# Kernel tuning notes

Hardware: AMD Instinct MI355X
Metric: run time of the kernel (lower is better)

Reference implementation:

```python
import jax, jax.numpy as jnp
import numpy as np

T_VALUES = [0.015, 0.06, 0.25, 1.0]
EPS = 1e-05
SR_OVER_HOP = 44100.0 / 512.0  # frames per second


def _s_values():
    t = np.asarray(T_VALUES, dtype=np.float32) * SR_OVER_HOP
    s = (np.sqrt(1.0 + 4.0 * t ** 2) - 1.0) / (2.0 * t ** 2)
    return jnp.asarray(s, dtype=jnp.float32)  # (n_s,)


def setup_inputs() -> dict:
    key = jax.random.key(0)
    k1, = jax.random.split(key, 1)
    B, F, T = 16, 128, 4096
    # non-negative energies (spectrogram magnitudes)
    x = jax.random.uniform(k1, (B, F, T), dtype=jnp.float32) * 10.0
    alpha_log = jnp.full((F,), float(np.log(0.8)), dtype=jnp.float32)
    delta_log = jnp.full((F,), float(np.log(10.0)), dtype=jnp.float32)
    r_log = jnp.full((F,), float(np.log(0.25)), dtype=jnp.float32)
    return {"x": x, "alpha_log": alpha_log, "delta_log": delta_log, "r_log": r_log}


def reference(x, alpha_log, delta_log, r_log):
    # x: (B, F, T)
    s = _s_values()                      # (n_s,)
    s_b = s[:, None, None]               # (n_s, 1, 1)
    B, F, T = x.shape
    n_s = s.shape[0]

    # Multi-rate EMA over time (first-order IIR), init with first frame.
    xs = jnp.moveaxis(x, -1, 0)          # (T, B, F)
    m0 = jnp.broadcast_to(xs[0][None], (n_s, B, F))

    def step(m, xt):
        m = (1.0 - s_b) * m + s_b * xt[None]  # (n_s, B, F)
        return m, m

    _, m_rest = jax.lax.scan(step, m0, xs[1:])          # (T-1, n_s, B, F)
    m_seq = jnp.concatenate([m0[None], m_rest], axis=0)  # (T, n_s, B, F)
    smoother = jnp.moveaxis(m_seq, 0, -1)                # (n_s, B, F, T)

    alpha = jnp.exp(alpha_log)[None, None, :, None]      # per band
    delta = jnp.exp(delta_log)[None, None, :, None]
    r = jnp.exp(r_log)[None, None, :, None]

    log_eps = jnp.log(jnp.asarray(EPS, dtype=x.dtype))
    smooth = jnp.exp(-alpha * (log_eps + jnp.log1p(smoother / EPS)))
    pcen = (x[None] * smooth + delta) ** r - delta ** r   # (n_s, B, F, T)
    return jnp.transpose(pcen, (1, 0, 2, 3))              # (B, n_s, F, T)
```

## Files before the change

kernel.cpp:

```cpp
#include <hip/hip_runtime.h>


#define EPS_C 1e-5f

__device__ __forceinline__ float fexp2(float v) { return __builtin_amdgcn_exp2f(v); }
__device__ __forceinline__ float flog2(float v) { return __builtin_amdgcn_logf(v); }
__device__ __forceinline__ float fpow(float a, float b) { return fexp2(b * flog2(a)); }
__device__ __forceinline__ float fexp(float v) { return fexp2(v * 1.44269504f); }

__global__ __launch_bounds__(1024)
void pcen_kernel(const float* __restrict__ x,
                 const float* __restrict__ alpha_log,
                 const float* __restrict__ delta_log,
                 const float* __restrict__ r_log,
                 float* __restrict__ out)
{
    const int row  = blockIdx.x;
    const int f    = row & 127;
    const int b    = row >> 7;
    const int tid  = threadIdx.x;
    const int lane = tid & 63;
    const int w    = tid >> 6;

    __shared__ float wq[4][16];
    __shared__ float sh_x0;

    const float4* __restrict__ xrow4 = (const float4*)(x + (size_t)row * 4096);
    float4 xv = xrow4[tid];
    if (tid == 0) sh_x0 = xv.x;

    const float Tv[4] = {0.015f, 0.06f, 0.25f, 1.0f};
    float s_arr[4], omn_arr[4];
#pragma unroll
    for (int i = 0; i < 4; ++i) {
        float t  = Tv[i] * 86.1328125f;
        float t2 = t * t;
        float s  = (__builtin_sqrtf(1.0f + 4.0f * t2) - 1.0f) / (2.0f * t2);
        s_arr[i]   = s;
        omn_arr[i] = 1.0f - s;
    }

    float qxv[4];
#pragma unroll
    for (int i = 0; i < 4; ++i) {
        const float s = s_arr[i], omn = omn_arr[i];
        float p = s * xv.x;
        p = fmaf(omn, p, s * xv.y);
        p = fmaf(omn, p, s * xv.z);
        p = fmaf(omn, p, s * xv.w);
        float q = p;
        float c = omn * omn; c = c * c;
#pragma unroll
        for (int k = 0; k < 6; ++k) {
            int d = 1 << k;
            float tsh = __shfl_up(q, d);
            if (lane >= d) q = fmaf(c, tsh, q);
            c = c * c;
        }
        float qx = __shfl_up(q, 1);
        if (lane == 0) qx = 0.0f;
        qxv[i] = qx;
        if (lane == 63) wq[i][w] = q;
    }
    __syncthreads();

    const float al = alpha_log[f], dl = delta_log[f], rl = r_log[f];
    const float nalpha  = -fexp(al);
    const float delta   =  fexp(dl);
    const float r       =  fexp(rl);
    const float delta_r =  fexp(r * dl);

    const float x0 = sh_x0;
    float4* __restrict__ out4 = (float4*)out;

#pragma unroll
    for (int i = 0; i < 4; ++i) {
        const float s = s_arr[i], omn = omn_arr[i];
        const float l2omn = flog2(omn);
        const float Dw = fexp2(256.0f * l2omn);
        float Q = x0;
        for (int v = 0; v < w; ++v) Q = fmaf(Dw, Q, wq[i][v]);
        const float dl4 = fexp2((float)(4 * lane) * l2omn);
        const float E = fmaf(dl4, Q, qxv[i]);
        float m0 = fmaf(omn, E,  s * xv.x);
        float m1 = fmaf(omn, m0, s * xv.y);
        float m2 = fmaf(omn, m1, s * xv.z);
        float m3 = fmaf(omn, m2, s * xv.w);
        float4 o;
        o.x = fpow(fmaf(xv.x, fpow(EPS_C + m0, nalpha), delta), r) - delta_r;
        o.y = fpow(fmaf(xv.y, fpow(EPS_C + m1, nalpha), delta), r) - delta_r;
        o.z = fpow(fmaf(xv.z, fpow(EPS_C + m2, nalpha), delta), r) - delta_r;
        o.w = fpow(fmaf(xv.w, fpow(EPS_C + m3, nalpha), delta), r) - delta_r;

        const size_t obase4 = ((size_t)((b * 4 + i) * 128 + f)) * 1024;
        out4[obase4 + tid] = o;
    }
}

extern "C" void kernel_launch(void* const* d_in, const int* in_sizes, int n_in,
                              void* d_out, int out_size, void* d_ws, size_t ws_size,
                              hipStream_t stream) {
    const float* x  = (const float*)d_in[0];
    const float* al = (const float*)d_in[1];
    const float* dl = (const float*)d_in[2];
    const float* rl = (const float*)d_in[3];
    float* out = (float*)d_out;
    const int rows = in_sizes[0] / 4096;
    pcen_kernel<<<rows, 1024, 0, stream>>>(x, al, dl, rl, out);
}
```

Baseline: 164.7 us.

## Process sixteen elements per thread with 256-thread blocks for PCEN scan

```diff
diff --git a/kernel.cpp b/kernel.cpp
--- a/kernel.cpp
+++ b/kernel.cpp
@@ -8,7 +8,7 @@
 __device__ __forceinline__ float fpow(float a, float b) { return fexp2(b * flog2(a)); }
 __device__ __forceinline__ float fexp(float v) { return fexp2(v * 1.44269504f); }
 
-__global__ __launch_bounds__(1024)
+__global__ __launch_bounds__(256, 6)
 void pcen_kernel(const float* __restrict__ x,
                  const float* __restrict__ alpha_log,
                  const float* __restrict__ delta_log,
@@ -22,12 +22,17 @@
     const int lane = tid & 63;
     const int w    = tid >> 6;
 
-    __shared__ float wq[4][16];
+    __shared__ float wq[4][4];
     __shared__ float sh_x0;
 
     const float4* __restrict__ xrow4 = (const float4*)(x + (size_t)row * 4096);
-    float4 xv = xrow4[tid];
-    if (tid == 0) sh_x0 = xv.x;
+    float xs[16];
+#pragma unroll
+    for (int k = 0; k < 4; ++k) {
+        float4 v = xrow4[4 * tid + k];
+        xs[4*k+0] = v.x; xs[4*k+1] = v.y; xs[4*k+2] = v.z; xs[4*k+3] = v.w;
+    }
+    if (tid == 0) sh_x0 = xs[0];
 
     const float Tv[4] = {0.015f, 0.06f, 0.25f, 1.0f};
     float s_arr[4], omn_arr[4];
@@ -44,12 +49,12 @@
 #pragma unroll
     for (int i = 0; i < 4; ++i) {
         const float s = s_arr[i], omn = omn_arr[i];
-        float p = s * xv.x;
-        p = fmaf(omn, p, s * xv.y);
-        p = fmaf(omn, p, s * xv.z);
-        p = fmaf(omn, p, s * xv.w);
+        float p = 0.0f;
+#pragma unroll
+        for (int j = 0; j < 16; ++j) p = fmaf(omn, p, s * xs[j]);
+        float c = omn * omn;
+        c = c * c; c = c * c; c = c * c;
         float q = p;
-        float c = omn * omn; c = c * c;
 #pragma unroll
         for (int k = 0; k < 6; ++k) {
             int d = 1 << k;
@@ -62,38 +67,41 @@
         qxv[i] = qx;
         if (lane == 63) wq[i][w] = q;
     }
+
+    const float al = alpha_log[f], dlg = delta_log[f], rl = r_log[f];
+    const float nalpha  = -fexp(al);
+    const float delta   =  fexp(dlg);
+    const float r       =  fexp(rl);
+    const float delta_r =  fexp(r * dlg);
+
     __syncthreads();
+    const float x0 = sh_x0;
 
-    const float al = alpha_log[f], dl = delta_log[f], rl = r_log[f];
-    const float nalpha  = -fexp(al);
-    const float delta   =  fexp(dl);
-    const float r       =  fexp(rl);
-    const float delta_r =  fexp(r * dl);
-
-    const float x0 = sh_x0;
     float4* __restrict__ out4 = (float4*)out;
 
 #pragma unroll
     for (int i = 0; i < 4; ++i) {
         const float s = s_arr[i], omn = omn_arr[i];
         const float l2omn = flog2(omn);
-        const float Dw = fexp2(256.0f * l2omn);
+        const float Dw = fexp2(1024.0f * l2omn);
         float Q = x0;
         for (int v = 0; v < w; ++v) Q = fmaf(Dw, Q, wq[i][v]);
-        const float dl4 = fexp2((float)(4 * lane) * l2omn);
-        const float E = fmaf(dl4, Q, qxv[i]);
-        float m0 = fmaf(omn, E,  s * xv.x);
-        float m1 = fmaf(omn, m0, s * xv.y);
-        float m2 = fmaf(omn, m1, s * xv.z);
-        float m3 = fmaf(omn, m2, s * xv.w);
-        float4 o;
-        o.x = fpow(fmaf(xv.x, fpow(EPS_C + m0, nalpha), delta), r) - delta_r;
-        o.y = fpow(fmaf(xv.y, fpow(EPS_C + m1, nalpha), delta), r) - delta_r;
-        o.z = fpow(fmaf(xv.z, fpow(EPS_C + m2, nalpha), delta), r) - delta_r;
-        o.w = fpow(fmaf(xv.w, fpow(EPS_C + m3, nalpha), delta), r) - delta_r;
-
-        const size_t obase4 = ((size_t)((b * 4 + i) * 128 + f)) * 1024;
-        out4[obase4 + tid] = o;
+        const float dlane = fexp2((float)(16 * lane) * l2omn);
+        float m = fmaf(dlane, Q, qxv[i]);
+        const size_t obase4 = ((size_t)((b * 4 + i) * 128 + f)) * 1024 + 4 * tid;
+#pragma unroll
+        for (int k = 0; k < 4; ++k) {
+            float4 o;
+            m = fmaf(omn, m, s * xs[4*k+0]);
+            o.x = fpow(fmaf(xs[4*k+0], fpow(EPS_C + m, nalpha), delta), r) - delta_r;
+            m = fmaf(omn, m, s * xs[4*k+1]);
+            o.y = fpow(fmaf(xs[4*k+1], fpow(EPS_C + m, nalpha), delta), r) - delta_r;
+            m = fmaf(omn, m, s * xs[4*k+2]);
+            o.z = fpow(fmaf(xs[4*k+2], fpow(EPS_C + m, nalpha), delta), r) - delta_r;
+            m = fmaf(omn, m, s * xs[4*k+3]);
+            o.w = fpow(fmaf(xs[4*k+3], fpow(EPS_C + m, nalpha), delta), r) - delta_r;
+            out4[obase4 + k] = o;
+        }
     }
 }
 
@@ -106,5 +114,5 @@
     const float* rl = (const float*)d_in[3];
     float* out = (float*)d_out;
     const int rows = in_sizes[0] / 4096;
-    pcen_kernel<<<rows, 1024, 0, stream>>>(x, al, dl, rl, out);
+    pcen_kernel<<<rows, 256, 0, stream>>>(x, al, dl, rl, out);
 }
```

Measured after the change: 177.9 us. 8.0% more time.
